# Performance work log

Hardware: AMD Instinct MI355X
Metric: run time of the kernel (lower is better)

## Reference

```python
import jax, jax.numpy as jnp
import numpy as np

N_NODES = 50000
N_EDGES = 400000
IN, HID, OUT = 256, 64, 64
HEADS = (8, 8, 1)
NEG_SLOPE = 0.2


def setup_inputs() -> dict:
    key = jax.random.key(0)
    ks = jax.random.split(key, 16)
    def lin(k, fi, fo):
        return jax.random.normal(k, (fi, fo), jnp.float32) / np.sqrt(fi)
    H0, H1, H2 = HEADS
    return {
        "x": jax.random.normal(ks[0], (N_NODES, IN), jnp.float32),
        "src": jax.random.randint(ks[1], (N_EDGES,), 0, N_NODES),
        "dst": jax.random.randint(ks[2], (N_EDGES,), 0, N_NODES),
        # layer 0: in=256 -> (8 heads, 64)
        "W1": lin(ks[3], IN, H0 * HID),
        "al1": 0.1 * jax.random.normal(ks[4], (H0, HID), jnp.float32),
        "ar1": 0.1 * jax.random.normal(ks[5], (H0, HID), jnp.float32),
        "b1": jnp.zeros((H0 * HID,), jnp.float32),
        # layer 1: in=512 -> (8 heads, 64), identity residual (512 == 8*64)
        "W2": lin(ks[6], H0 * HID, H1 * HID),
        "al2": 0.1 * jax.random.normal(ks[7], (H1, HID), jnp.float32),
        "ar2": 0.1 * jax.random.normal(ks[8], (H1, HID), jnp.float32),
        "b2": jnp.zeros((H1 * HID,), jnp.float32),
        # layer 2: in=512 -> (1 head, 64), linear residual projection
        "W3": lin(ks[9], H1 * HID, H2 * OUT),
        "al3": 0.1 * jax.random.normal(ks[10], (H2, OUT), jnp.float32),
        "ar3": 0.1 * jax.random.normal(ks[11], (H2, OUT), jnp.float32),
        "b3": jnp.zeros((H2 * OUT,), jnp.float32),
        "Wr3": lin(ks[12], H1 * HID, H2 * OUT),
    }


def _gat_conv(h, src, dst, W, al, ar, b, res, act):
    # DGL GATConv on a homogeneous graph (feat_src == feat_dst).
    N = h.shape[0]
    H, D = al.shape
    f = (h @ W).reshape(N, H, D)                       # [N,H,D]
    el = jnp.sum(f * al[None], axis=-1)                # [N,H]
    er = jnp.sum(f * ar[None], axis=-1)                # [N,H]
    e = jax.nn.leaky_relu(el[src] + er[dst], NEG_SLOPE)  # [E,H]
    # segment softmax over incoming edges of each dst node
    m = jax.ops.segment_max(e, dst, num_segments=N)    # [N,H]
    ex = jnp.exp(e - m[dst])
    denom = jax.ops.segment_sum(ex, dst, num_segments=N)
    alpha = ex / denom[dst]                            # [E,H]
    msg = f[src] * alpha[:, :, None]                   # [E,H,D]
    rst = jax.ops.segment_sum(msg, dst, num_segments=N)  # [N,H,D]
    if res is not None:
        rst = rst + res
    rst = rst + b.reshape(1, H, D)
    return act(rst) if act is not None else rst


def reference(x, src, dst, W1, al1, ar1, b1, W2, al2, ar2, b2,
              W3, al3, ar3, b3, Wr3):
    N = x.shape[0]
    h = _gat_conv(x, src, dst, W1, al1, ar1, b1, None, jax.nn.elu)
    h = h.reshape(N, -1)                               # flatten(1)
    res2 = h.reshape(N, HEADS[1], HID)                 # identity residual
    h = _gat_conv(h, src, dst, W2, al2, ar2, b2, res2, jax.nn.elu)
    h = h.reshape(N, -1)
    res3 = (h @ Wr3).reshape(N, HEADS[2], OUT)         # projected residual
    h = _gat_conv(h, src, dst, W3, al3, ar3, b3, res3, None)
    return h.mean(axis=1)                              # mean over heads
```

## Files before the change

### kernel.cpp

```cpp
#include <hip/hip_runtime.h>
#include <hip/hip_bf16.h>

#define N_NODES 50000
#define M_PAD 50048
#define N_EDGES 400000
#define SCAN_B 256

typedef __attribute__((ext_vector_type(8))) short short8;
typedef __attribute__((ext_vector_type(4))) float f32x4;

__device__ __forceinline__ float b2f(unsigned short u) {
    return __uint_as_float(((unsigned)u) << 16);
}
__device__ __forceinline__ unsigned short f2b(float f) {
    unsigned u = __float_as_uint(f);
    return (unsigned short)((u + 0x7fffu + ((u >> 16) & 1u)) >> 16);
}
__device__ __forceinline__ float blo(unsigned u) { return __uint_as_float(u << 16); }
__device__ __forceinline__ float bhi(unsigned u) { return __uint_as_float(u & 0xffff0000u); }

__device__ __forceinline__ void gload_lds16(const void* g, void* l) {
    __builtin_amdgcn_global_load_lds(
        (const __attribute__((address_space(1))) unsigned int*)g,
        (__attribute__((address_space(3))) unsigned int*)l, 16, 0, 0);
}

#define X4_N (N_NODES * 64)
#define W1_SZ (512 * 256)
#define W2_SZ (512 * 512)
#define W3_SZ (64 * 512)
__global__ __launch_bounds__(256) void prep_k(const float* __restrict__ x,
                                              const float* __restrict__ W1,
                                              const float* __restrict__ W2,
                                              const float* __restrict__ W3,
                                              const float* __restrict__ Wr3,
                                              unsigned short* __restrict__ xb,
                                              unsigned short* __restrict__ Wt1,
                                              unsigned short* __restrict__ Wt2,
                                              unsigned short* __restrict__ Wt3) {
    int i = blockIdx.x * blockDim.x + threadIdx.x;
    if (i < X4_N) {
        float4 v = *(const float4*)&x[(size_t)i * 4];
        unsigned short o[4] = {f2b(v.x), f2b(v.y), f2b(v.z), f2b(v.w)};
        *(ushort2*)&xb[(size_t)i * 4] = make_ushort2(o[0], o[1]);
        *(ushort2*)&xb[(size_t)i * 4 + 2] = make_ushort2(o[2], o[3]);
        return;
    }
    int o = i - X4_N;
    if (o < W1_SZ) {
        int n = o / 256, k = o % 256;
        Wt1[o] = f2b(W1[(size_t)k * 512 + n]);
    } else if (o < W1_SZ + W2_SZ) {
        int oo = o - W1_SZ;
        int n = oo / 512, k = oo % 512;
        Wt2[oo] = f2b(W2[(size_t)k * 512 + n]);
    } else if (o < W1_SZ + W2_SZ + W3_SZ) {
        int oo = o - W1_SZ - W2_SZ;
        int n = oo / 512, k = oo % 512;
        Wt3[oo] = f2b(W3[(size_t)k * 64 + n]);
    } else if (o < W1_SZ + W2_SZ + 2 * W3_SZ) {
        int oo = o - W1_SZ - W2_SZ - W3_SZ;
        int n = oo / 512, k = oo % 512;
        Wt3[W3_SZ + oo] = f2b(Wr3[(size_t)k * 64 + n]);
    }
}

template <int H, bool ELER>
__global__ __launch_bounds__(256, 2) void gemm_mfma(const unsigned short* __restrict__ A,
                                                    const unsigned short* __restrict__ Bt,
                                                    unsigned short* __restrict__ C,
                                                    const float* __restrict__ al,
                                                    const float* __restrict__ ar,
                                                    float* __restrict__ el,
                                                    float* __restrict__ er,
                                                    int M, int NN, int K) {
    __shared__ unsigned short As[128 * 32];
    __shared__ unsigned short Bs[128 * 32];
    const int tid = threadIdx.x;
    const int w = tid >> 6, l = tid & 63;
    const int bm = blockIdx.y * 128, bn = blockIdx.x * 128;
    const int wr = w >> 1, wc = w & 1;
    const int rA = l >> 2;
    const int kA = (l & 3) * 8;
    const int fr = l & 15, fq = l >> 4;
    f32x4 acc[4][4] = {};

    for (int k0 = 0; k0 < K; k0 += 32) {
#pragma unroll
        for (int j = 0; j < 2; ++j) {
            int row = w * 32 + j * 16 + rA;
            gload_lds16(&A[(size_t)(bm + row) * K + k0 + kA], &As[(w * 2 + j) * 512]);
            gload_lds16(&Bt[(size_t)(bn + row) * K + k0 + kA], &Bs[(w * 2 + j) * 512]);
        }
        __syncthreads();
        short8 a[4], b[4];
#pragma unroll
        for (int m = 0; m < 4; ++m)
            a[m] = *(const short8*)&As[(wr * 64 + m * 16 + fr) * 32 + fq * 8];
#pragma unroll
        for (int n = 0; n < 4; ++n)
            b[n] = *(const short8*)&Bs[(wc * 64 + n * 16 + fr) * 32 + fq * 8];
#pragma unroll
        for (int m = 0; m < 4; ++m)
#pragma unroll
            for (int n = 0; n < 4; ++n)
                acc[m][n] = __builtin_amdgcn_mfma_f32_16x16x32_bf16(a[m], b[n], acc[m][n], 0, 0, 0);
        __syncthreads();
    }

    if (ELER) {
        const int head = (bn >> 6) + wc;
        if (head < H) {
            float alv[4], arv[4];
#pragma unroll
            for (int n = 0; n < 4; ++n) {
                alv[n] = al[head * 64 + n * 16 + fr];
                arv[n] = ar[head * 64 + n * 16 + fr];
            }
#pragma unroll
            for (int m = 0; m < 4; ++m) {
#pragma unroll
                for (int j = 0; j < 4; ++j) {
                    float pl = acc[m][0][j] * alv[0] + acc[m][1][j] * alv[1] +
                               acc[m][2][j] * alv[2] + acc[m][3][j] * alv[3];
                    float pr = acc[m][0][j] * arv[0] + acc[m][1][j] * arv[1] +
                               acc[m][2][j] * arv[2] + acc[m][3][j] * arv[3];
#pragma unroll
                    for (int off = 1; off < 16; off <<= 1) {
                        pl += __shfl_xor(pl, off);
                        pr += __shfl_xor(pr, off);
                    }
                    int r = bm + wr * 64 + m * 16 + fq * 4 + j;
                    if (fr == 0 && r < M) {
                        el[(size_t)r * H + head] = pl;
                        er[(size_t)r * H + head] = pr;
                    }
                }
            }
        }
    }

#pragma unroll
    for (int m = 0; m < 4; ++m) {
#pragma unroll
        for (int j = 0; j < 4; ++j) {
            int r = bm + wr * 64 + m * 16 + fq * 4 + j;
            if (r < M) {
#pragma unroll
                for (int n = 0; n < 4; ++n)
                    C[(size_t)r * NN + bn + wc * 64 + n * 16 + fr] = f2b(acc[m][n][j]);
            }
        }
    }
}

__global__ __launch_bounds__(256) void hist_k(const int* __restrict__ dst,
                                              int* __restrict__ deg, int E) {
    int i = blockIdx.x * blockDim.x + threadIdx.x;
    if (i < E) atomicAdd(&deg[dst[i]], 1);
}

__global__ __launch_bounds__(SCAN_B) void scan_blocks(const int* __restrict__ in,
                                                      int* __restrict__ out,
                                                      int* __restrict__ part, int n) {
    __shared__ int tmp[SCAN_B];
    int t = threadIdx.x, g = blockIdx.x * SCAN_B + t;
    int v = (g < n) ? in[g] : 0;
    tmp[t] = v;
    __syncthreads();
    for (int off = 1; off < SCAN_B; off <<= 1) {
        int add = (t >= off) ? tmp[t - off] : 0;
        __syncthreads();
        tmp[t] += add;
        __syncthreads();
    }
    if (g < n) out[g] = tmp[t] - v;
    if (t == SCAN_B - 1) part[blockIdx.x] = tmp[t];
}

__global__ __launch_bounds__(SCAN_B) void scan_part(int* __restrict__ part, int n) {
    __shared__ int tmp[SCAN_B];
    int t = threadIdx.x;
    int v = (t < n) ? part[t] : 0;
    tmp[t] = v;
    __syncthreads();
    for (int off = 1; off < SCAN_B; off <<= 1) {
        int add = (t >= off) ? tmp[t - off] : 0;
        __syncthreads();
        tmp[t] += add;
        __syncthreads();
    }
    if (t < n) part[t] = tmp[t] - v;
}

__global__ __launch_bounds__(256) void add_off(int* __restrict__ rowptr,
                                               int* __restrict__ cursor,
                                               const int* __restrict__ part,
                                               int n, int E) {
    int g = blockIdx.x * blockDim.x + threadIdx.x;
    if (g < n) {
        int v = rowptr[g] + part[g / SCAN_B];
        rowptr[g] = v;
        cursor[g] = v;
    }
    if (g == 0) rowptr[n] = E;
}

__global__ __launch_bounds__(256) void scatter_k(const int* __restrict__ src,
                                                 const int* __restrict__ dst,
                                                 int* __restrict__ cursor,
                                                 int* __restrict__ csr_src, int E) {
    int e = blockIdx.x * blockDim.x + threadIdx.x;
    if (e < E) {
        int p = atomicAdd(&cursor[dst[e]], 1);
        csr_src[p] = src[e];
    }
}

template <bool HAS_INIT>
__global__ __launch_bounds__(256) void gat_agg8(const unsigned short* __restrict__ f,
                                                const float* __restrict__ el,
                                                const float* __restrict__ er,
                                                const int* __restrict__ rowptr,
                                                const int* __restrict__ csr_src,
                                                const unsigned short* __restrict__ init,
                                                const float* __restrict__ bias,
                                                unsigned short* __restrict__ outb, int N) {
    int w = (blockIdx.x * blockDim.x + threadIdx.x) >> 6;
    int lane = threadIdx.x & 63;
    if (w >= N) return;
    const int d = w;
    const int s0 = rowptr[d], s1 = rowptr[d + 1];
    const int hh = lane & 7;
    const int esub = lane >> 3;
    const int myhead = lane >> 3;
    const int sl8 = lane * 8;
    const float erh = er[(size_t)d * 8 + hh];

    int i0 = s0 + esub;
    bool valid0 = i0 < s1;
    int sn0 = csr_src[valid0 ? i0 : s0];
    uint4 pk[8];
#pragma unroll
    for (int j = 0; j < 8; ++j) {
        int snj = __shfl(sn0, j << 3);
        pk[j] = *(const uint4*)&f[(size_t)snj * 512 + sl8];
    }

    float v0 = el[(size_t)sn0 * 8 + hh] + erh;
    v0 = v0 > 0.f ? v0 : 0.2f * v0;
    float mx = valid0 ? v0 : -1e30f;
    for (int i = s0 + 8 + esub; i < s1; i += 8) {
        float v = el[(size_t)csr_src[i] * 8 + hh] + erh;
        v = v > 0.f ? v : 0.2f * v;
        mx = fmaxf(mx, v);
    }
    mx = fmaxf(mx, __shfl_xor(mx, 8));
    mx = fmaxf(mx, __shfl_xor(mx, 16));
    mx = fmaxf(mx, __shfl_xor(mx, 32));

    float am0 = valid0 ? __expf(v0 - mx) : 0.f;
    float sm = am0;
    float acc[8] = {};
#pragma unroll
    for (int j = 0; j < 8; ++j) {
        float alpha = __shfl(am0, (j << 3) | myhead);
        acc[0] += blo(pk[j].x) * alpha;
        acc[1] += bhi(pk[j].x) * alpha;
        acc[2] += blo(pk[j].y) * alpha;
        acc[3] += bhi(pk[j].y) * alpha;
        acc[4] += blo(pk[j].z) * alpha;
        acc[5] += bhi(pk[j].z) * alpha;
        acc[6] += blo(pk[j].w) * alpha;
        acc[7] += bhi(pk[j].w) * alpha;
    }

    for (int ii = s0 + 8; ii < s1; ii += 8) {
        int i = ii + esub;
        bool valid = i < s1;
        int sn_mine = csr_src[valid ? i : s0];
        uint4 qk[8];
#pragma unroll
        for (int j = 0; j < 8; ++j) {
            int snj = __shfl(sn_mine, j << 3);
            qk[j] = *(const uint4*)&f[(size_t)snj * 512 + sl8];
        }
        float v = el[(size_t)sn_mine * 8 + hh] + erh;
        v = v > 0.f ? v : 0.2f * v;
        float am = valid ? __expf(v - mx) : 0.f;
        sm += am;
#pragma unroll
        for (int j = 0; j < 8; ++j) {
            float alpha = __shfl(am, (j << 3) | myhead);
            acc[0] += blo(qk[j].x) * alpha;
            acc[1] += bhi(qk[j].x) * alpha;
            acc[2] += blo(qk[j].y) * alpha;
            acc[3] += bhi(qk[j].y) * alpha;
            acc[4] += blo(qk[j].z) * alpha;
            acc[5] += bhi(qk[j].z) * alpha;
            acc[6] += blo(qk[j].w) * alpha;
            acc[7] += bhi(qk[j].w) * alpha;
        }
    }

    sm += __shfl_xor(sm, 8);
    sm += __shfl_xor(sm, 16);
    sm += __shfl_xor(sm, 32);
    float smh = __shfl(sm, myhead);
    float inv = smh > 0.f ? 1.0f / smh : 0.f;
#pragma unroll
    for (int j = 0; j < 8; ++j) acc[j] *= inv;

    const int sl = (lane & 7) * 8;
    float4 b0 = *(const float4*)&bias[myhead * 64 + sl];
    float4 b1 = *(const float4*)&bias[myhead * 64 + sl + 4];
    float bb[8] = {b0.x, b0.y, b0.z, b0.w, b1.x, b1.y, b1.z, b1.w};
    if (HAS_INIT) {
        uint4 iv = *(const uint4*)&init[(size_t)d * 512 + sl8];
        acc[0] += blo(iv.x); acc[1] += bhi(iv.x);
        acc[2] += blo(iv.y); acc[3] += bhi(iv.y);
        acc[4] += blo(iv.z); acc[5] += bhi(iv.z);
        acc[6] += blo(iv.w); acc[7] += bhi(iv.w);
    }
    unsigned short ob[8];
#pragma unroll
    for (int j = 0; j < 8; ++j) {
        float v = acc[j] + bb[j];
        v = v > 0.f ? v : __expf(v) - 1.f;
        ob[j] = f2b(v);
    }
    uint4 ov;
    ov.x = (unsigned)ob[0] | ((unsigned)ob[1] << 16);
    ov.y = (unsigned)ob[2] | ((unsigned)ob[3] << 16);
    ov.z = (unsigned)ob[4] | ((unsigned)ob[5] << 16);
    ov.w = (unsigned)ob[6] | ((unsigned)ob[7] << 16);
    *(uint4*)&outb[(size_t)d * 512 + sl8] = ov;
}

__global__ __launch_bounds__(256) void gat_agg1(const unsigned short* __restrict__ f,
                                                const float* __restrict__ el,
                                                const float* __restrict__ er,
                                                const int* __restrict__ rowptr,
                                                const int* __restrict__ csr_src,
                                                const float* __restrict__ bias,
                                                float* __restrict__ outf, int N) {
    int w = (blockIdx.x * blockDim.x + threadIdx.x) >> 6;
    int lane = threadIdx.x & 63;
    if (w >= N) return;
    const int d = w;
    const int s0 = rowptr[d], s1 = rowptr[d + 1];
    const int esub = lane >> 3, sl = (lane & 7) * 8;
    const float erh = er[d];

    int i0 = s0 + esub;
    bool valid0 = i0 < s1;
    int sn0 = csr_src[valid0 ? i0 : s0];
    uint4 pk0 = *(const uint4*)&f[(size_t)sn0 * 128 + sl];

    float v0 = el[sn0] + erh;
    v0 = v0 > 0.f ? v0 : 0.2f * v0;
    float mx = valid0 ? v0 : -1e30f;
    for (int i = s0 + 8 + esub; i < s1; i += 8) {
        float v = el[csr_src[i]] + erh;
        v = v > 0.f ? v : 0.2f * v;
        mx = fmaxf(mx, v);
    }
    mx = fmaxf(mx, __shfl_xor(mx, 8));
    mx = fmaxf(mx, __shfl_xor(mx, 16));
    mx = fmaxf(mx, __shfl_xor(mx, 32));

    float am0 = valid0 ? __expf(v0 - mx) : 0.f;
    float sm = am0;
    float acc[8];
    acc[0] = blo(pk0.x) * am0; acc[1] = bhi(pk0.x) * am0;
    acc[2] = blo(pk0.y) * am0; acc[3] = bhi(pk0.y) * am0;
    acc[4] = blo(pk0.z) * am0; acc[5] = bhi(pk0.z) * am0;
    acc[6] = blo(pk0.w) * am0; acc[7] = bhi(pk0.w) * am0;

    for (int ii = s0 + 8; ii < s1; ii += 8) {
        int i = ii + esub;
        bool valid = i < s1;
        int sn = csr_src[valid ? i : s0];
        uint4 pk = *(const uint4*)&f[(size_t)sn * 128 + sl];
        float v = el[sn] + erh;
        v = v > 0.f ? v : 0.2f * v;
        float am = valid ? __expf(v - mx) : 0.f;
        sm += am;
        acc[0] += blo(pk.x) * am; acc[1] += bhi(pk.x) * am;
        acc[2] += blo(pk.y) * am; acc[3] += bhi(pk.y) * am;
        acc[4] += blo(pk.z) * am; acc[5] += bhi(pk.z) * am;
        acc[6] += blo(pk.w) * am; acc[7] += bhi(pk.w) * am;
    }

    sm += __shfl_xor(sm, 8);
    sm += __shfl_xor(sm, 16);
    sm += __shfl_xor(sm, 32);
#pragma unroll
    for (int off = 8; off < 64; off <<= 1)
#pragma unroll
        for (int j = 0; j < 8; ++j) acc[j] += __shfl_xor(acc[j], off);
    float inv = sm > 0.f ? 1.0f / sm : 0.f;

    if (esub == 0) {
        uint4 rv = *(const uint4*)&f[(size_t)d * 128 + 64 + sl];
        float rr[8] = {blo(rv.x), bhi(rv.x), blo(rv.y), bhi(rv.y),
                       blo(rv.z), bhi(rv.z), blo(rv.w), bhi(rv.w)};
#pragma unroll
        for (int j = 0; j < 8; ++j)
            outf[(size_t)d * 64 + sl + j] = acc[j] * inv + bias[sl + j] + rr[j];
    }
}

extern "C" void kernel_launch(void* const* d_in, const int* in_sizes, int n_in,
                              void* d_out, int out_size, void* d_ws, size_t ws_size,
                              hipStream_t stream) {
    const float* x   = (const float*)d_in[0];
    const int*   src = (const int*)d_in[1];
    const int*   dst = (const int*)d_in[2];
    const float* W1  = (const float*)d_in[3];
    const float* al1 = (const float*)d_in[4];
    const float* ar1 = (const float*)d_in[5];
    const float* b1  = (const float*)d_in[6];
    const float* W2  = (const float*)d_in[7];
    const float* al2 = (const float*)d_in[8];
    const float* ar2 = (const float*)d_in[9];
    const float* b2  = (const float*)d_in[10];
    const float* W3  = (const float*)d_in[11];
    const float* al3 = (const float*)d_in[12];
    const float* ar3 = (const float*)d_in[13];
    const float* b3  = (const float*)d_in[14];
    const float* Wr3 = (const float*)d_in[15];
    float* out = (float*)d_out;

    unsigned short* xb   = (unsigned short*)d_ws;
    unsigned short* fb   = xb + (size_t)M_PAD * 256;
    unsigned short* h1b  = fb + (size_t)M_PAD * 512;
    unsigned short* h2b  = h1b + (size_t)M_PAD * 512;
    unsigned short* f3r  = h2b + (size_t)M_PAD * 512;
    unsigned short* Wt1  = f3r + (size_t)M_PAD * 128;
    unsigned short* Wt2  = Wt1 + 512 * 256;
    unsigned short* Wt3  = Wt2 + 512 * 512;
    float* el = (float*)(Wt3 + 128 * 512);
    float* er = el + (size_t)N_NODES * 8;
    int* rowptr  = (int*)(er + (size_t)N_NODES * 8);
    int* cursor  = rowptr + (N_NODES + 1);
    int* part    = cursor + N_NODES;
    int* csr_src = part + 256;

    const dim3 blk(256);
    const int E = N_EDGES, N = N_NODES;
    const int nb = (N + SCAN_B - 1) / SCAN_B;
    const int gy = (N + 127) / 128;

    prep_k<<<(X4_N + W1_SZ + W2_SZ + 2 * W3_SZ + 255) / 256, blk, 0, stream>>>(
        x, W1, W2, W3, Wr3, xb, Wt1, Wt2, Wt3);

    hipMemsetAsync(cursor, 0, (size_t)N * 4, stream);
    hipMemsetAsync(csr_src + E, 0, 8 * 4, stream);
    hist_k<<<(E + 255) / 256, blk, 0, stream>>>(dst, cursor, E);
    scan_blocks<<<nb, SCAN_B, 0, stream>>>(cursor, rowptr, part, N);
    scan_part<<<1, SCAN_B, 0, stream>>>(part, nb);
    add_off<<<nb, blk, 0, stream>>>(rowptr, cursor, part, N, E);
    scatter_k<<<(E + 255) / 256, blk, 0, stream>>>(src, dst, cursor, csr_src, E);

    gemm_mfma<8, true><<<dim3(4, gy), blk, 0, stream>>>(
        xb, Wt1, fb, al1, ar1, el, er, N, 512, 256);
    gat_agg8<false><<<(N + 3) / 4, blk, 0, stream>>>(
        fb, el, er, rowptr, csr_src, nullptr, b1, h1b, N);

    gemm_mfma<8, true><<<dim3(4, gy), blk, 0, stream>>>(
        h1b, Wt2, fb, al2, ar2, el, er, N, 512, 512);
    gat_agg8<true><<<(N + 3) / 4, blk, 0, stream>>>(
        fb, el, er, rowptr, csr_src, h1b, b2, h2b, N);

    gemm_mfma<1, true><<<dim3(1, gy), blk, 0, stream>>>(
        h2b, Wt3, f3r, al3, ar3, el, er, N, 128, 512);
    gat_agg1<<<(N + 3) / 4, blk, 0, stream>>>(
        f3r, el, er, rowptr, csr_src, b3, out, N);
}
```

Before: 357.0 us.

## Fuse histogram into prep kernel, swizzle GEMM blocks, and load CSR indices directly

Folds the degree histogram into the prep kernel and moves the csr_src padding zeroing into add_off. This removes a separate launch and a memset. GEMM launches become 1D with a swizzled block order that groups 8 row tiles across the 4 column tiles, aiming for better L2 reuse of A rows. The aggregation kernels now read the 8 neighbour indices directly from csr_src instead of broadcasting them via shuffles, with out-of-range entries pointing at a zero padding slot. This trades a few redundant index loads for fewer cross-lane ops.

Result: faster. 343.7 us (-3.7%).

```diff
diff --git a/kernel.cpp b/kernel.cpp
--- a/kernel.cpp
+++ b/kernel.cpp
@@ -9,9 +9,6 @@
 typedef __attribute__((ext_vector_type(8))) short short8;
 typedef __attribute__((ext_vector_type(4))) float f32x4;
 
-__device__ __forceinline__ float b2f(unsigned short u) {
-    return __uint_as_float(((unsigned)u) << 16);
-}
 __device__ __forceinline__ unsigned short f2b(float f) {
     unsigned u = __float_as_uint(f);
     return (unsigned short)((u + 0x7fffu + ((u >> 16) & 1u)) >> 16);
@@ -29,15 +26,18 @@
 #define W1_SZ (512 * 256)
 #define W2_SZ (512 * 512)
 #define W3_SZ (64 * 512)
+#define WTOT (W1_SZ + W2_SZ + 2 * W3_SZ)
 __global__ __launch_bounds__(256) void prep_k(const float* __restrict__ x,
                                               const float* __restrict__ W1,
                                               const float* __restrict__ W2,
                                               const float* __restrict__ W3,
                                               const float* __restrict__ Wr3,
+                                              const int* __restrict__ dst,
                                               unsigned short* __restrict__ xb,
                                               unsigned short* __restrict__ Wt1,
                                               unsigned short* __restrict__ Wt2,
-                                              unsigned short* __restrict__ Wt3) {
+                                              unsigned short* __restrict__ Wt3,
+                                              int* __restrict__ deg) {
     int i = blockIdx.x * blockDim.x + threadIdx.x;
     if (i < X4_N) {
         float4 v = *(const float4*)&x[(size_t)i * 4];
@@ -58,14 +58,17 @@
         int oo = o - W1_SZ - W2_SZ;
         int n = oo / 512, k = oo % 512;
         Wt3[oo] = f2b(W3[(size_t)k * 64 + n]);
-    } else if (o < W1_SZ + W2_SZ + 2 * W3_SZ) {
+    } else if (o < WTOT) {
         int oo = o - W1_SZ - W2_SZ - W3_SZ;
         int n = oo / 512, k = oo % 512;
         Wt3[W3_SZ + oo] = f2b(Wr3[(size_t)k * 64 + n]);
-    }
-}
-
-template <int H, bool ELER>
+    } else {
+        int e = o - WTOT;
+        if (e < N_EDGES) atomicAdd(&deg[dst[e]], 1);
+    }
+}
+
+template <int H, int NBX, bool ELER>
 __global__ __launch_bounds__(256, 2) void gemm_mfma(const unsigned short* __restrict__ A,
                                                     const unsigned short* __restrict__ Bt,
                                                     unsigned short* __restrict__ C,
@@ -74,11 +77,29 @@
                                                     float* __restrict__ el,
                                                     float* __restrict__ er,
                                                     int M, int NN, int K) {
+    const int nby = (M + 127) >> 7;
+    int bid = blockIdx.x;
+    int r, c;
+    if (NBX == 4) {
+        int full = nby & ~7;
+        int nfull = full * 4;
+        if (bid < nfull) {
+            r = (bid >> 5) * 8 + (bid & 7);
+            c = (bid >> 3) & 3;
+        } else {
+            int t = bid - nfull, rem = nby - full;
+            r = full + t % rem;
+            c = t / rem;
+        }
+    } else {
+        r = bid;
+        c = 0;
+    }
     __shared__ unsigned short As[128 * 32];
     __shared__ unsigned short Bs[128 * 32];
     const int tid = threadIdx.x;
     const int w = tid >> 6, l = tid & 63;
-    const int bm = blockIdx.y * 128, bn = blockIdx.x * 128;
+    const int bm = r * 128, bn = c * 128;
     const int wr = w >> 1, wc = w & 1;
     const int rA = l >> 2;
     const int kA = (l & 3) * 8;
@@ -130,10 +151,10 @@
                         pl += __shfl_xor(pl, off);
                         pr += __shfl_xor(pr, off);
                     }
-                    int r = bm + wr * 64 + m * 16 + fq * 4 + j;
-                    if (fr == 0 && r < M) {
-                        el[(size_t)r * H + head] = pl;
-                        er[(size_t)r * H + head] = pr;
+                    int rr = bm + wr * 64 + m * 16 + fq * 4 + j;
+                    if (fr == 0 && rr < M) {
+                        el[(size_t)rr * H + head] = pl;
+                        er[(size_t)rr * H + head] = pr;
                     }
                 }
             }
@@ -144,20 +165,14 @@
     for (int m = 0; m < 4; ++m) {
 #pragma unroll
         for (int j = 0; j < 4; ++j) {
-            int r = bm + wr * 64 + m * 16 + fq * 4 + j;
-            if (r < M) {
+            int rr = bm + wr * 64 + m * 16 + fq * 4 + j;
+            if (rr < M) {
 #pragma unroll
                 for (int n = 0; n < 4; ++n)
-                    C[(size_t)r * NN + bn + wc * 64 + n * 16 + fr] = f2b(acc[m][n][j]);
+                    C[(size_t)rr * NN + bn + wc * 64 + n * 16 + fr] = f2b(acc[m][n][j]);
             }
         }
     }
-}
-
-__global__ __launch_bounds__(256) void hist_k(const int* __restrict__ dst,
-                                              int* __restrict__ deg, int E) {
-    int i = blockIdx.x * blockDim.x + threadIdx.x;
-    if (i < E) atomicAdd(&deg[dst[i]], 1);
 }
 
 __global__ __launch_bounds__(SCAN_B) void scan_blocks(const int* __restrict__ in,
@@ -196,6 +211,7 @@
 __global__ __launch_bounds__(256) void add_off(int* __restrict__ rowptr,
                                                int* __restrict__ cursor,
                                                const int* __restrict__ part,
+                                               int* __restrict__ csr_src,
                                                int n, int E) {
     int g = blockIdx.x * blockDim.x + threadIdx.x;
     if (g < n) {
@@ -204,6 +220,7 @@
         cursor[g] = v;
     }
     if (g == 0) rowptr[n] = E;
+    if (g < 8) csr_src[E + g] = 0;
 }
 
 __global__ __launch_bounds__(256) void scatter_k(const int* __restrict__ src,
@@ -237,17 +254,17 @@
     const int sl8 = lane * 8;
     const float erh = er[(size_t)d * 8 + hh];
 
-    int i0 = s0 + esub;
-    bool valid0 = i0 < s1;
-    int sn0 = csr_src[valid0 ? i0 : s0];
+    int snj[8];
+#pragma unroll
+    for (int j = 0; j < 8; ++j)
+        snj[j] = csr_src[(s0 + j < s1) ? (s0 + j) : N_EDGES];
     uint4 pk[8];
 #pragma unroll
-    for (int j = 0; j < 8; ++j) {
-        int snj = __shfl(sn0, j << 3);
-        pk[j] = *(const uint4*)&f[(size_t)snj * 512 + sl8];
-    }
-
-    float v0 = el[(size_t)sn0 * 8 + hh] + erh;
+    for (int j = 0; j < 8; ++j)
+        pk[j] = *(const uint4*)&f[(size_t)snj[j] * 512 + sl8];
+
+    bool valid0 = s0 + esub < s1;
+    float v0 = el[(size_t)snj[esub] * 8 + hh] + erh;
     v0 = v0 > 0.f ? v0 : 0.2f * v0;
     float mx = valid0 ? v0 : -1e30f;
     for (int i = s0 + 8 + esub; i < s1; i += 8) {
@@ -276,16 +293,16 @@
     }
 
     for (int ii = s0 + 8; ii < s1; ii += 8) {
-        int i = ii + esub;
-        bool valid = i < s1;
-        int sn_mine = csr_src[valid ? i : s0];
+        int sn2[8];
+#pragma unroll
+        for (int j = 0; j < 8; ++j)
+            sn2[j] = csr_src[(ii + j < s1) ? (ii + j) : N_EDGES];
         uint4 qk[8];
 #pragma unroll
-        for (int j = 0; j < 8; ++j) {
-            int snj = __shfl(sn_mine, j << 3);
-            qk[j] = *(const uint4*)&f[(size_t)snj * 512 + sl8];
-        }
-        float v = el[(size_t)sn_mine * 8 + hh] + erh;
+        for (int j = 0; j < 8; ++j)
+            qk[j] = *(const uint4*)&f[(size_t)sn2[j] * 512 + sl8];
+        bool valid = ii + esub < s1;
+        float v = el[(size_t)sn2[esub] * 8 + hh] + erh;
         v = v > 0.f ? v : 0.2f * v;
         float am = valid ? __expf(v - mx) : 0.f;
         sm += am;
@@ -352,11 +369,14 @@
     const int esub = lane >> 3, sl = (lane & 7) * 8;
     const float erh = er[d];
 
-    int i0 = s0 + esub;
-    bool valid0 = i0 < s1;
-    int sn0 = csr_src[valid0 ? i0 : s0];
+    int snj[8];
+#pragma unroll
+    for (int j = 0; j < 8; ++j)
+        snj[j] = csr_src[(s0 + j < s1) ? (s0 + j) : N_EDGES];
+    int sn0 = snj[esub];
     uint4 pk0 = *(const uint4*)&f[(size_t)sn0 * 128 + sl];
 
+    bool valid0 = s0 + esub < s1;
     float v0 = el[sn0] + erh;
     v0 = v0 > 0.f ? v0 : 0.2f * v0;
     float mx = valid0 ? v0 : -1e30f;
@@ -380,7 +400,7 @@
     for (int ii = s0 + 8; ii < s1; ii += 8) {
         int i = ii + esub;
         bool valid = i < s1;
-        int sn = csr_src[valid ? i : s0];
+        int sn = csr_src[valid ? i : N_EDGES];
         uint4 pk = *(const uint4*)&f[(size_t)sn * 128 + sl];
         float v = el[sn] + erh;
         v = v > 0.f ? v : 0.2f * v;
@@ -452,28 +472,25 @@
     const int nb = (N + SCAN_B - 1) / SCAN_B;
     const int gy = (N + 127) / 128;
 
-    prep_k<<<(X4_N + W1_SZ + W2_SZ + 2 * W3_SZ + 255) / 256, blk, 0, stream>>>(
-        x, W1, W2, W3, Wr3, xb, Wt1, Wt2, Wt3);
-
     hipMemsetAsync(cursor, 0, (size_t)N * 4, stream);
-    hipMemsetAsync(csr_src + E, 0, 8 * 4, stream);
-    hist_k<<<(E + 255) / 256, blk, 0, stream>>>(dst, cursor, E);
+    prep_k<<<(X4_N + WTOT + E + 255) / 256, blk, 0, stream>>>(
+        x, W1, W2, W3, Wr3, dst, xb, Wt1, Wt2, Wt3, cursor);
     scan_blocks<<<nb, SCAN_B, 0, stream>>>(cursor, rowptr, part, N);
     scan_part<<<1, SCAN_B, 0, stream>>>(part, nb);
-    add_off<<<nb, blk, 0, stream>>>(rowptr, cursor, part, N, E);
+    add_off<<<nb, blk, 0, stream>>>(rowptr, cursor, part, csr_src, N, E);
     scatter_k<<<(E + 255) / 256, blk, 0, stream>>>(src, dst, cursor, csr_src, E);
 
-    gemm_mfma<8, true><<<dim3(4, gy), blk, 0, stream>>>(
+    gemm_mfma<8, 4, true><<<4 * gy, blk, 0, stream>>>(
         xb, Wt1, fb, al1, ar1, el, er, N, 512, 256);
     gat_agg8<false><<<(N + 3) / 4, blk, 0, stream>>>(
         fb, el, er, rowptr, csr_src, nullptr, b1, h1b, N);
 
-    gemm_mfma<8, true><<<dim3(4, gy), blk, 0, stream>>>(
+    gemm_mfma<8, 4, true><<<4 * gy, blk, 0, stream>>>(
         h1b, Wt2, fb, al2, ar2, el, er, N, 512, 512);
     gat_agg8<true><<<(N + 3) / 4, blk, 0, stream>>>(
         fb, el, er, rowptr, csr_src, h1b, b2, h2b, N);
 
-    gemm_mfma<1, true><<<dim3(1, gy), blk, 0, stream>>>(
+    gemm_mfma<1, 1, true><<<gy, blk, 0, stream>>>(
         h2b, Wt3, f3r, al3, ar3, el, er, N, 128, 512);
     gat_agg1<<<(N + 3) / 4, blk, 0, stream>>>(
         f3r, el, er, rowptr, csr_src, b3, out, N);
```
